# Kernel optimization log

Hardware: AMD Instinct MI355X
Metric: run time of the kernel (lower is better)

## Reference

```python
import jax, jax.numpy as jnp
import numpy as np
import math

B, S, HID = 2, 2048, 1152
NH, NKV = 16, 4
HD = HID // NH  # 72
GROUPS = NH // NKV  # 4
ROPE_BASE = 10000.0


def setup_inputs() -> dict:
    key = jax.random.key(0)
    ks = jax.random.split(key, 5)
    hidden_states = jax.random.normal(ks[0], (B, S, HID), dtype=jnp.float32)
    # causal additive mask: 0 on/below diagonal, -1e9 above
    causal = jnp.tril(jnp.ones((S, S), dtype=jnp.bool_))
    attention_mask = jnp.where(causal, 0.0, -1e9).astype(jnp.float32)[None, None]
    scale = 0.02
    wq = jax.random.normal(ks[1], (HID, HID), dtype=jnp.float32) * scale
    wk = jax.random.normal(ks[2], (NKV * HD, HID), dtype=jnp.float32) * scale
    wv = jax.random.normal(ks[3], (NKV * HD, HID), dtype=jnp.float32) * scale
    wo = jax.random.normal(ks[4], (HID, HID), dtype=jnp.float32) * scale
    return {"hidden_states": hidden_states, "attention_mask": attention_mask,
            "wq": wq, "wk": wk, "wv": wv, "wo": wo}


def _rotate_half(x):
    x1, x2 = jnp.split(x, 2, axis=-1)
    return jnp.concatenate((-x2, x1), axis=-1)


def _rope_cos_sin(seq_len, dim, dtype):
    inv_freq = 1.0 / (ROPE_BASE ** (jnp.arange(0, dim, 2, dtype=jnp.float32) / dim))
    t = jnp.arange(seq_len, dtype=jnp.float32)
    freqs = jnp.outer(t, inv_freq)          # [S, dim/2]
    emb = jnp.concatenate((freqs, freqs), axis=-1)  # [S, dim]
    return jnp.cos(emb).astype(dtype), jnp.sin(emb).astype(dtype)


def reference(hidden_states, attention_mask, wq, wk, wv, wo):
    b, s, _ = hidden_states.shape
    # projections (nn.Linear: x @ W.T)
    q = (hidden_states @ wq.T).reshape(b, s, NH, HD).transpose(0, 2, 1, 3)    # [b,nh,s,hd]
    k = (hidden_states @ wk.T).reshape(b, s, NKV, HD).transpose(0, 2, 1, 3)   # [b,nkv,s,hd]
    v = (hidden_states @ wv.T).reshape(b, s, NKV, HD).transpose(0, 2, 1, 3)
    # RoPE
    cos, sin = _rope_cos_sin(s, HD, hidden_states.dtype)
    cos, sin = cos[None, None], sin[None, None]  # [1,1,s,hd]
    q = q * cos + _rotate_half(q) * sin
    k = k * cos + _rotate_half(k) * sin
    # expand kv heads (repeat_interleave over head dim)
    k = jnp.repeat(k, GROUPS, axis=1)  # [b,nh,s,hd]
    v = jnp.repeat(v, GROUPS, axis=1)
    scores = jnp.einsum('bhqd,bhkd->bhqk', q, k) / math.sqrt(HD)
    scores = scores + attention_mask
    attn = jax.nn.softmax(scores.astype(jnp.float32), axis=-1).astype(q.dtype)
    out = jnp.einsum('bhqk,bhkd->bhqd', attn, v)
    out = out.transpose(0, 2, 1, 3).reshape(b, s, HID)
    return out @ wo.T
```

## Files before the change

### kernel.cpp

```cpp
#include <hip/hip_runtime.h>
#include <hip/hip_bf16.h>
#include <cstddef>

#define B_   2
#define S_   2048
#define HID_ 1152
#define NH_  16
#define NKV_ 4
#define HD_  72
#define MTOT (B_ * S_)
#define KVDIM (NKV_ * HD_)

typedef float f32x4 __attribute__((ext_vector_type(4)));
typedef short bf16x8 __attribute__((ext_vector_type(8)));
typedef short s4v __attribute__((ext_vector_type(4)));

__device__ __forceinline__ float bf2f(short x) {
  unsigned int u = ((unsigned int)(unsigned short)x) << 16;
  return __builtin_bit_cast(float, u);
}
__device__ __forceinline__ short f2bf(float f) {
  unsigned int u = __builtin_bit_cast(unsigned int, f);
  u += 0x7fff + ((u >> 16) & 1);
  return (short)(u >> 16);
}

__device__ __forceinline__ float fast_exp2(float x) {
#if __has_builtin(__builtin_amdgcn_exp2f)
  return __builtin_amdgcn_exp2f(x);
#else
  return exp2f(x);
#endif
}

__device__ __forceinline__ void async16(const short* g, short* lds) {
  __builtin_amdgcn_global_load_lds((const __attribute__((address_space(1))) void*)g,
                                   (__attribute__((address_space(3))) void*)lds,
                                   16, 0, 0);
}

__global__ void k_cvt_all(const float4* __restrict__ s0, const float4* __restrict__ s1,
                          const float4* __restrict__ s2, const float4* __restrict__ s3,
                          const float4* __restrict__ s4,
                          s4v* __restrict__ d0, s4v* __restrict__ d1, s4v* __restrict__ d2,
                          s4v* __restrict__ d3, s4v* __restrict__ d4,
                          float2* __restrict__ tab, short* __restrict__ Vt,
                          int n0, int n1, int n2, int n3, int n4t) {
  int ncvt = n0 + n1 + n2 + n3 + n4t;
  int ntab = S_ * 36;
  int total = ncvt + ntab + 32768;
  for (int i = blockIdx.x * blockDim.x + threadIdx.x; i < total;
       i += gridDim.x * blockDim.x) {
    if (i < ncvt) {
      const float4* s;
      s4v* d;
      int off = i;
      bool perm = false;
      if (off < n0) { s = s0; d = d0; }
      else {
        off -= n0;
        if (off < n1) { s = s1; d = d1; perm = true; }
        else {
          off -= n1;
          if (off < n2) { s = s2; d = d2; perm = true; }
          else {
            off -= n2;
            if (off < n3) { s = s3; d = d3; }
            else { off -= n3; s = s4; d = d4; }
          }
        }
      }
      float4 v = s[off];
      s4v o = { f2bf(v.x), f2bf(v.y), f2bf(v.z), f2bf(v.w) };
      int out = off;
      if (perm) {
        int r = off / 288, k4 = off - r * 288;
        int hh = r / 72, ii = r - hh * 72;
        int pr = hh * 72 + (ii < 36 ? 2 * ii : 2 * (ii - 36) + 1);
        out = pr * 288 + k4;
      }
      d[out] = o;
    } else if (i < ncvt + ntab) {
      int idx = i - ncvt;
      int ii = idx % 36, s = idx / 36;
      float freq = powf(10000.0f, -(float)ii / 36.0f);
      float a = (float)s * freq;
      tab[idx] = make_float2(cosf(a), sinf(a));
    } else {
      int idx2 = i - ncvt - ntab;
      int t = idx2 << 2;
      int sp = t & 2047;
      int rest = t >> 11;
      int dr = rest & 7;
      int bkv = rest >> 3;
      s4v val = {};
      if (dr == 0) { val[0] = (short)0x3F80; val[1] = (short)0x3F80;
                     val[2] = (short)0x3F80; val[3] = (short)0x3F80; }
      *(s4v*)(Vt + (size_t)bkv * 163840 + (size_t)(72 + dr) * 2048 + sp) = val;
    }
  }
}

#define BM 128
#define BN 128
#define BK 32

__global__ __launch_bounds__(256) void k_gemm_qkv(const short* __restrict__ A,
                                                  const short* __restrict__ Wq,
                                                  const short* __restrict__ Wk,
                                                  const short* __restrict__ Wv,
                                                  short* __restrict__ Qo,
                                                  short* __restrict__ Ko,
                                                  short* __restrict__ Vt,
                                                  const float2* __restrict__ tab) {
  const int K = HID_, NTOT = 1728;
  __shared__ short smem[16384];
  short* As0 = smem;
  short* Bs0 = smem + 4096;
  short* As1 = smem + 8192;
  short* Bs1 = smem + 12288;
  const int tid = threadIdx.x;
  const int l = tid & 63;
  const int w = tid >> 6;
  const int bm = blockIdx.x * BM;
  const int bn = blockIdx.y * BN;
  const int wr = (w >> 1) * 64;
  const int wc = (w & 1) * 64;
  const int c15 = l & 15, g = l >> 4;
  const int r0 = tid >> 2;
  const int c0 = (tid & 3) * 8;

  const short* srcA[2];
  const short* srcB[2];
#pragma unroll
  for (int it = 0; it < 2; ++it) {
    int ar = bm + it * 64 + r0;
    int br = bn + it * 64 + r0;
    if (br > NTOT - 1) br = NTOT - 1;
    const short* bsrc;
    if (br < 1152)      bsrc = Wq + (size_t)br * K;
    else if (br < 1440) bsrc = Wk + (size_t)(br - 1152) * K;
    else                bsrc = Wv + (size_t)(br - 1440) * K;
    srcA[it] = A + (size_t)ar * K + c0;
    srcB[it] = bsrc + c0;
  }

  auto STAGE = [&](short* Ad, short* Bd) {
#pragma unroll
    for (int it = 0; it < 2; ++it) {
      async16(srcA[it], &Ad[(it * 64 + r0) * BK + c0]);
      async16(srcB[it], &Bd[(it * 64 + r0) * BK + c0]);
      srcA[it] += BK;
      srcB[it] += BK;
    }
  };

  f32x4 acc[4][4] = {};

  STAGE(As0, Bs0);
  short *Ac = As0, *Bc = Bs0, *An = As1, *Bn = Bs1;

  for (int k0 = 0; k0 < K; k0 += BK) {
    asm volatile("s_waitcnt vmcnt(0)" ::: "memory");
    __builtin_amdgcn_sched_barrier(0);
    __syncthreads();
    if (k0 + BK < K) STAGE(An, Bn);

    bf16x8 af[4], bfr[4];
#pragma unroll
    for (int t = 0; t < 4; ++t) {
      af[t]  = *(const bf16x8*)&Ac[(wr + t * 16 + c15) * BK + g * 8];
      bfr[t] = *(const bf16x8*)&Bc[(wc + t * 16 + c15) * BK + g * 8];
    }
#pragma unroll
    for (int mt = 0; mt < 4; ++mt)
#pragma unroll
      for (int nt = 0; nt < 4; ++nt)
        acc[mt][nt] = __builtin_amdgcn_mfma_f32_16x16x32_bf16(af[mt], bfr[nt], acc[mt][nt], 0, 0, 0);

    short* t1 = Ac; Ac = An; An = t1;
    short* t2 = Bc; Bc = Bn; Bn = t2;
  }

#pragma unroll
  for (int mt = 0; mt < 4; ++mt)
#pragma unroll
    for (int nt = 0; nt < 4; ++nt) {
      int col = bn + wc + nt * 16 + c15;
      if (col < 1152) {
#pragma unroll
        for (int j = 0; j < 4; ++j) {
          int row = bm + wr + mt * 16 + g * 4 + j;
          Qo[(size_t)row * HID_ + col] = f2bf(acc[mt][nt][j]);
        }
      } else if (col < 1440) {
        int ch = col - 1152;
        int ii = (ch % 72) >> 1;
#pragma unroll
        for (int j = 0; j < 4; ++j) {
          int row = bm + wr + mt * 16 + g * 4 + j;
          float v = acc[mt][nt][j];
          float p = __shfl_xor(v, 1);
          float2 cs = tab[(size_t)(row & (S_ - 1)) * 36 + ii];
          float r = (c15 & 1) ? (v * cs.x + p * cs.y)
                              : (v * cs.x - p * cs.y);
          Ko[(size_t)row * KVDIM + ch] = f2bf(r);
        }
      } else if (col < NTOT) {
        int cv = col - 1440;
        int d = cv % 72, kvh = cv / 72;
        int row0 = bm + wr + mt * 16 + g * 4;
        int bkv = (row0 >> 11) * 4 + kvh;
        s4v out;
#pragma unroll
        for (int j = 0; j < 4; ++j) out[j] = f2bf(acc[mt][nt][j]);
        *(s4v*)(Vt + (size_t)bkv * 163840 + (size_t)d * 2048 + (row0 & 2047)) = out;
      }
    }
}

__global__ __launch_bounds__(256) void k_gemm_o(const short* __restrict__ A,
                                                const short* __restrict__ Bm,
                                                float* __restrict__ C,
                                                int M, int N, int K) {
  __shared__ short smem[16384];
  short* As0 = smem;
  short* Bs0 = smem + 4096;
  short* As1 = smem + 8192;
  short* Bs1 = smem + 12288;
  const int tid = threadIdx.x;
  const int l = tid & 63;
  const int w = tid >> 6;
  const int bm = blockIdx.x * BM;
  const int bn = blockIdx.y * BN;
  const int wr = (w >> 1) * 64;
  const int wc = (w & 1) * 64;
  const int c15 = l & 15, g = l >> 4;
  const int r0 = tid >> 2;
  const int c0 = (tid & 3) * 8;

  const short* srcA[2];
  const short* srcB[2];
#pragma unroll
  for (int it = 0; it < 2; ++it) {
    int ar = bm + it * 64 + r0;
    int br = bn + it * 64 + r0;
    if (br > N - 1) br = N - 1;
    srcA[it] = A + (size_t)ar * K + c0;
    srcB[it] = Bm + (size_t)br * K + c0;
  }

  auto STAGE = [&](short* Ad, short* Bd) {
#pragma unroll
    for (int it = 0; it < 2; ++it) {
      async16(srcA[it], &Ad[(it * 64 + r0) * BK + c0]);
      async16(srcB[it], &Bd[(it * 64 + r0) * BK + c0]);
      srcA[it] += BK;
      srcB[it] += BK;
    }
  };

  f32x4 acc[4][4] = {};

  STAGE(As0, Bs0);
  short *Ac = As0, *Bc = Bs0, *An = As1, *Bn = Bs1;

  for (int k0 = 0; k0 < K; k0 += BK) {
    asm volatile("s_waitcnt vmcnt(0)" ::: "memory");
    __builtin_amdgcn_sched_barrier(0);
    __syncthreads();
    if (k0 + BK < K) STAGE(An, Bn);

    bf16x8 af[4], bfr[4];
#pragma unroll
    for (int t = 0; t < 4; ++t) {
      af[t]  = *(const bf16x8*)&Ac[(wr + t * 16 + c15) * BK + g * 8];
      bfr[t] = *(const bf16x8*)&Bc[(wc + t * 16 + c15) * BK + g * 8];
    }
#pragma unroll
    for (int mt = 0; mt < 4; ++mt)
#pragma unroll
      for (int nt = 0; nt < 4; ++nt)
        acc[mt][nt] = __builtin_amdgcn_mfma_f32_16x16x32_bf16(af[mt], bfr[nt], acc[mt][nt], 0, 0, 0);

    short* t1 = Ac; Ac = An; An = t1;
    short* t2 = Bc; Bc = Bn; Bn = t2;
  }

#pragma unroll
  for (int mt = 0; mt < 4; ++mt)
#pragma unroll
    for (int nt = 0; nt < 4; ++nt)
#pragma unroll
      for (int j = 0; j < 4; ++j) {
        int row = bm + wr + mt * 16 + g * 4 + j;
        int col = bn + wc + nt * 16 + c15;
        if (col < N) C[(size_t)row * N + col] = acc[mt][nt][j];
      }
}

#define QB 16
#define KT 64

__global__ __launch_bounds__(256, 2) void k_flash(const short* __restrict__ Q,
                                                  const short* __restrict__ Kg,
                                                  const short* __restrict__ Vt,
                                                  short* __restrict__ O,
                                                  const float2* __restrict__ tab) {
  const int bid = blockIdx.x;
  const int bkv = bid & 7;
  const int qt = 127 - (bid >> 3);
  const int b = bkv >> 2, kv = bkv & 3;
  const int tid = threadIdx.x;
  const int w = tid >> 6, l = tid & 63;
  const int h = kv * 4 + w;
  const int q0 = qt * QB;
  const int c15 = l & 15, g = l >> 4;

  __shared__ short lds[24064];
  short* Ks0 = lds;
  short* Ks1 = lds + 9728;
  short* Ps  = lds + 19456 + w * 1152;

  const float SCL = 0.117851130f * 1.4426950408889634f;
  const float SHIFT = 8.0f;

  const short* Qbase = Q + (size_t)(b * S_) * HID_ + h * HD_;
  const short* Kbase = Kg + (size_t)(b * S_) * KVDIM + kv * HD_;
  const short* Vbase = Vt + (size_t)bkv * 80 * S_;

  const short* gk[3];
  const short* gv[3];
  int lk[3], lv[3];
  bool vkf[3], vvf[3];
#pragma unroll
  for (int i = 0; i < 3; ++i) {
    int c = tid + 256 * i;
    vkf[i] = c < 576;
    int row = c / 9, cc = c - row * 9;
    if (row > 63) row = 63;
    gk[i] = Kbase + (size_t)row * KVDIM + cc * 8;
    lk[i] = c < 576 ? c * 8 : 0;
    int c2 = tid + 256 * i;
    vvf[i] = c2 < 640;
    int vrow = (c2 >> 3) & 127, slot = c2 & 7;
    if (vrow > 79) vrow = 79;
    gv[i] = Vbase + (size_t)vrow * S_ + ((slot ^ (vrow & 7)) << 3);
    lv[i] = c2 < 640 ? c2 * 8 : 0;
  }

  const int lane_k = c15 * 72 + g * 8;
  const short* rKa = Ks0 + lane_k;
  const short* rKb = Ks1 + lane_k;
  const int lane_v0 = 4608 + c15 * 64 + ((g ^ (c15 & 7)) << 3);
  const int lane_v1 = 4608 + c15 * 64 + (((4 + g) ^ (c15 & 7)) << 3);
  const short* rV0a = lds + lane_v0;
  const short* rV0b = lds + 9728 + lane_v0;
  const short* rV1a = lds + lane_v1;
  const short* rV1b = lds + 9728 + lane_v1;
  short* pPw = Ps + g * 288 + c15;
  const short* pPr = Ps + c15 * 72 + g * 8;

  bf16x8 qf[3];
  const bf16x8 zfrag = {0, 0, 0, 0, 0, 0, 0, 0};
  {
    int row = q0 + c15;
    const short* qrow = Qbase + (size_t)row * HID_;
    const float2* trow = tab + (size_t)row * 36;
#pragma unroll
    for (int ks = 0; ks < 3; ++ks) {
      int d0 = ks * 32 + g * 8;
      if (d0 < HD_) {
        bf16x8 raw = *(const bf16x8*)(qrow + d0);
        bf16x8 o;
#pragma unroll
        for (int e = 0; e < 8; e += 2) {
          float2 cs = trow[(d0 + e) >> 1];
          float x1 = bf2f(raw[e]), x2 = bf2f(raw[e + 1]);
          o[e]     = f2bf((x1 * cs.x - x2 * cs.y) * SCL);
          o[e + 1] = f2bf((x2 * cs.x + x1 * cs.y) * SCL);
        }
        qf[ks] = o;
      } else {
        qf[ks] = zfrag;
      }
    }
  }

  f32x4 accO[5] = {};

  const int nkt = (q0 + QB + KT - 1) / KT;
  const int nfull = (QB * qt + 1) >> 6;

  auto STAGE = [&](short* Kd, short* Vd) {
#pragma unroll
    for (int i = 0; i < 3; ++i) {
      if (vkf[i]) async16(gk[i], Kd + lk[i]);
      if (vvf[i]) async16(gv[i], Vd + lv[i]);
      gk[i] += KT * KVDIM;
      gv[i] += KT;
    }
  };

  STAGE(Ks0, lds + 4608);
  const short *rKc = rKa, *rKn = rKb;
  const short *rV0c = rV0a, *rV0n = rV0b;
  const short *rV1c = rV1a, *rV1n = rV1b;
  short *sKn = Ks1, *sVn = lds + 14336;
  short *sKc = Ks0, *sVc = lds + 4608;

  for (int kt = 0; kt < nkt; ++kt) {
    asm volatile("s_waitcnt vmcnt(0)" ::: "memory");
    __builtin_amdgcn_sched_barrier(0);
    __syncthreads();
    if (kt + 1 < nkt) STAGE(sKn, sVn);

    const int kbase = kt * KT;

    f32x4 sc[4] = {};
    __builtin_amdgcn_s_setprio(1);
#pragma unroll
    for (int ct = 0; ct < 4; ++ct)
#pragma unroll
      for (int ks = 0; ks < 3; ++ks) {
        bf16x8 kf = *(const bf16x8*)&rKc[ct * 1152 + ks * 32];
        sc[ct] = __builtin_amdgcn_mfma_f32_16x16x32_bf16(qf[ks], kf, sc[ct], 0, 0, 0);
      }
    __builtin_amdgcn_s_setprio(0);

    const int qrow = q0 + g * 4;
    if (kt >= nfull) {
#pragma unroll
      for (int ct = 0; ct < 4; ++ct) {
        int col = kbase + ct * 16 + c15;
#pragma unroll
        for (int j = 0; j < 4; ++j)
          if (col > qrow + j) sc[ct][j] = -1e30f;
      }
    }
#pragma unroll
    for (int ct = 0; ct < 4; ++ct)
#pragma unroll
      for (int j = 0; j < 4; ++j)
        sc[ct][j] = fast_exp2(sc[ct][j] - SHIFT);

#pragma unroll
    for (int ct = 0; ct < 4; ++ct)
#pragma unroll
      for (int j = 0; j < 4; ++j)
        pPw[j * 72 + ct * 16] = f2bf(sc[ct][j]);
    asm volatile("s_waitcnt lgkmcnt(0)" ::: "memory");
    __builtin_amdgcn_sched_barrier(0);
    bf16x8 pa0 = *(const bf16x8*)&pPr[0];
    bf16x8 pa1 = *(const bf16x8*)&pPr[32];

    __builtin_amdgcn_s_setprio(1);
#pragma unroll
    for (int dt = 0; dt < 5; ++dt) {
      bf16x8 vb0 = *(const bf16x8*)&rV0c[dt * 1024];
      bf16x8 vb1 = *(const bf16x8*)&rV1c[dt * 1024];
      accO[dt] = __builtin_amdgcn_mfma_f32_16x16x32_bf16(pa0, vb0, accO[dt], 0, 0, 0);
      accO[dt] = __builtin_amdgcn_mfma_f32_16x16x32_bf16(pa1, vb1, accO[dt], 0, 0, 0);
    }
    __builtin_amdgcn_s_setprio(0);

    const short* t;
    t = rKc; rKc = rKn; rKn = t;
    t = rV0c; rV0c = rV0n; rV0n = t;
    t = rV1c; rV1c = rV1n; rV1n = t;
    short* ts;
    ts = sKc; sKc = sKn; sKn = ts;
    ts = sVc; sVc = sVn; sVn = ts;
  }

  float lj[4];
#pragma unroll
  for (int j = 0; j < 4; ++j)
    lj[j] = 1.0f / __shfl(accO[4][j], (l & 48) | 8);
#pragma unroll
  for (int dt = 0; dt < 5; ++dt) {
    int d = dt * 16 + c15;
    if (d < HD_) {
#pragma unroll
      for (int j = 0; j < 4; ++j) {
        int row = q0 + g * 4 + j;
        O[(size_t)(b * S_ + row) * HID_ + h * HD_ + d] = f2bf(accO[dt][j] * lj[j]);
      }
    }
  }
}

extern "C" void kernel_launch(void* const* d_in, const int* in_sizes, int n_in,
                              void* d_out, int out_size, void* d_ws, size_t ws_size,
                              hipStream_t stream) {
  const float* hs = (const float*)d_in[0];
  const float* wq = (const float*)d_in[2];
  const float* wk = (const float*)d_in[3];
  const float* wv = (const float*)d_in[4];
  const float* wo = (const float*)d_in[5];

  char* ws = (char*)d_ws;
  short* Xb  = (short*)(ws + 0);
  short* Qb  = (short*)(ws + 9437184);
  short* Kb  = (short*)(ws + 18874368);
  short* Vt  = (short*)(ws + 23592960);
  short* Ob  = (short*)(ws + 26214400);
  short* wqb = (short*)(ws + 35651584);
  short* wkb = (short*)(ws + 38305792);
  short* wvb = (short*)(ws + 38969344);
  short* wob = (short*)(ws + 39632896);
  float2* tab = (float2*)(ws + 42287104);

  k_cvt_all<<<2048, 256, 0, stream>>>(
      (const float4*)hs, (const float4*)wq, (const float4*)wk, (const float4*)wv,
      (const float4*)wo,
      (s4v*)Xb, (s4v*)wqb, (s4v*)wkb, (s4v*)wvb, (s4v*)wob, tab, Vt,
      MTOT * HID_ / 4, HID_ * HID_ / 4, KVDIM * HID_ / 4, KVDIM * HID_ / 4,
      HID_ * HID_ / 4);

  k_gemm_qkv<<<dim3(32, 14), 256, 0, stream>>>(Xb, wqb, wkb, wvb, Qb, Kb, Vt, tab);

  k_flash<<<1024, 256, 0, stream>>>(Qb, Kb, Vt, Ob, tab);

  k_gemm_o<<<dim3(32, 9), 256, 0, stream>>>(Ob, wob, (float*)d_out, MTOT, HID_, HID_);
}
```

Measured before the change: 112.0 us.

## Double flash-attention key tile to 128 and reuse K buffer for probabilities

Raises the key/value tile size in the flash attention kernel from 64 to 128, so each iteration issues twice as many MFMAs per barrier and the loop runs half as many iterations. The P scratch area is dropped and probabilities are written into the just-consumed K tile, with an added __syncthreads before the writes. The V layout swizzle becomes 16-wide for 128-column rows. Staging addresses are recomputed each iteration instead of held in registers. LDS use grows, which may lower occupancy, and the causal tail does more masked wasted work per tile.

```diff
diff --git a/kernel.cpp b/kernel.cpp
--- a/kernel.cpp
+++ b/kernel.cpp
@@ -300,7 +300,7 @@
 }
 
 #define QB 16
-#define KT 64
+#define KT 128
 
 __global__ __launch_bounds__(256, 2) void k_flash(const short* __restrict__ Q,
                                                   const short* __restrict__ Kg,
@@ -317,10 +317,11 @@
   const int q0 = qt * QB;
   const int c15 = l & 15, g = l >> 4;
 
-  __shared__ short lds[24064];
+  __shared__ short lds[38912];
   short* Ks0 = lds;
-  short* Ks1 = lds + 9728;
-  short* Ps  = lds + 19456 + w * 1152;
+  short* Vs0 = lds + 9216;
+  short* Ks1 = lds + 19456;
+  short* Vs1 = lds + 28672;
 
   const float SCL = 0.117851130f * 1.4426950408889634f;
   const float SHIFT = 8.0f;
@@ -329,37 +330,14 @@
   const short* Kbase = Kg + (size_t)(b * S_) * KVDIM + kv * HD_;
   const short* Vbase = Vt + (size_t)bkv * 80 * S_;
 
-  const short* gk[3];
-  const short* gv[3];
-  int lk[3], lv[3];
-  bool vkf[3], vvf[3];
-#pragma unroll
-  for (int i = 0; i < 3; ++i) {
-    int c = tid + 256 * i;
-    vkf[i] = c < 576;
-    int row = c / 9, cc = c - row * 9;
-    if (row > 63) row = 63;
-    gk[i] = Kbase + (size_t)row * KVDIM + cc * 8;
-    lk[i] = c < 576 ? c * 8 : 0;
-    int c2 = tid + 256 * i;
-    vvf[i] = c2 < 640;
-    int vrow = (c2 >> 3) & 127, slot = c2 & 7;
-    if (vrow > 79) vrow = 79;
-    gv[i] = Vbase + (size_t)vrow * S_ + ((slot ^ (vrow & 7)) << 3);
-    lv[i] = c2 < 640 ? c2 * 8 : 0;
-  }
-
   const int lane_k = c15 * 72 + g * 8;
-  const short* rKa = Ks0 + lane_k;
-  const short* rKb = Ks1 + lane_k;
-  const int lane_v0 = 4608 + c15 * 64 + ((g ^ (c15 & 7)) << 3);
-  const int lane_v1 = 4608 + c15 * 64 + (((4 + g) ^ (c15 & 7)) << 3);
-  const short* rV0a = lds + lane_v0;
-  const short* rV0b = lds + 9728 + lane_v0;
-  const short* rV1a = lds + lane_v1;
-  const short* rV1b = lds + 9728 + lane_v1;
-  short* pPw = Ps + g * 288 + c15;
-  const short* pPr = Ps + c15 * 72 + g * 8;
+  int lane_v[4];
+#pragma unroll
+  for (int ks2 = 0; ks2 < 4; ++ks2)
+    lane_v[ks2] = c15 * 128 + (((ks2 * 4 + g) ^ c15) << 3);
+  const int pbase = w * 2176;
+  const int pw_off = pbase + (g * 4) * 136 + c15;
+  const int pr_off = pbase + c15 * 136 + g * 8;
 
   bf16x8 qf[3];
   const bf16x8 zfrag = {0, 0, 0, 0, 0, 0, 0, 0};
@@ -389,41 +367,44 @@
 
   f32x4 accO[5] = {};
 
-  const int nkt = (q0 + QB + KT - 1) / KT;
-  const int nfull = (QB * qt + 1) >> 6;
-
-  auto STAGE = [&](short* Kd, short* Vd) {
-#pragma unroll
-    for (int i = 0; i < 3; ++i) {
-      if (vkf[i]) async16(gk[i], Kd + lk[i]);
-      if (vvf[i]) async16(gv[i], Vd + lv[i]);
-      gk[i] += KT * KVDIM;
-      gv[i] += KT;
+  const int nkt = (16 * qt + 143) >> 7;
+  const int nfull = (16 * qt + 1) >> 7;
+
+  auto STAGE = [&](int kb, short* Kd, short* Vd) {
+    const short* kp = Kbase + (size_t)kb * KVDIM;
+    const short* vp = Vbase + kb;
+#pragma unroll
+    for (int i = 0; i < 10; ++i) {
+      int c = tid + 256 * i;
+      if (c < 1152) {
+        int row = c / 9, cc = c - row * 9;
+        async16(kp + (size_t)row * KVDIM + cc * 8, &Kd[c * 8]);
+      } else if (c < 2432) {
+        int c2 = c - 1152;
+        int row = c2 >> 4, slot = c2 & 15;
+        async16(vp + (size_t)row * S_ + ((slot ^ (row & 15)) << 3), &Vd[c2 * 8]);
+      }
     }
   };
 
-  STAGE(Ks0, lds + 4608);
-  const short *rKc = rKa, *rKn = rKb;
-  const short *rV0c = rV0a, *rV0n = rV0b;
-  const short *rV1c = rV1a, *rV1n = rV1b;
-  short *sKn = Ks1, *sVn = lds + 14336;
-  short *sKc = Ks0, *sVc = lds + 4608;
+  STAGE(0, Ks0, Vs0);
+  short *Ksc = Ks0, *Vsc = Vs0, *Ksn = Ks1, *Vsn = Vs1;
 
   for (int kt = 0; kt < nkt; ++kt) {
     asm volatile("s_waitcnt vmcnt(0)" ::: "memory");
     __builtin_amdgcn_sched_barrier(0);
     __syncthreads();
-    if (kt + 1 < nkt) STAGE(sKn, sVn);
+    if (kt + 1 < nkt) STAGE((kt + 1) * KT, Ksn, Vsn);
 
     const int kbase = kt * KT;
 
-    f32x4 sc[4] = {};
+    f32x4 sc[8] = {};
     __builtin_amdgcn_s_setprio(1);
 #pragma unroll
-    for (int ct = 0; ct < 4; ++ct)
+    for (int ct = 0; ct < 8; ++ct)
 #pragma unroll
       for (int ks = 0; ks < 3; ++ks) {
-        bf16x8 kf = *(const bf16x8*)&rKc[ct * 1152 + ks * 32];
+        bf16x8 kf = *(const bf16x8*)&Ksc[lane_k + ct * 1152 + ks * 32];
         sc[ct] = __builtin_amdgcn_mfma_f32_16x16x32_bf16(qf[ks], kf, sc[ct], 0, 0, 0);
       }
     __builtin_amdgcn_s_setprio(0);
@@ -431,7 +412,7 @@
     const int qrow = q0 + g * 4;
     if (kt >= nfull) {
 #pragma unroll
-      for (int ct = 0; ct < 4; ++ct) {
+      for (int ct = 0; ct < 8; ++ct) {
         int col = kbase + ct * 16 + c15;
 #pragma unroll
         for (int j = 0; j < 4; ++j)
@@ -439,38 +420,37 @@
       }
     }
 #pragma unroll
-    for (int ct = 0; ct < 4; ++ct)
+    for (int ct = 0; ct < 8; ++ct)
 #pragma unroll
       for (int j = 0; j < 4; ++j)
         sc[ct][j] = fast_exp2(sc[ct][j] - SHIFT);
 
-#pragma unroll
-    for (int ct = 0; ct < 4; ++ct)
+    __syncthreads();
+#pragma unroll
+    for (int ct = 0; ct < 8; ++ct)
 #pragma unroll
       for (int j = 0; j < 4; ++j)
-        pPw[j * 72 + ct * 16] = f2bf(sc[ct][j]);
+        Ksc[pw_off + j * 136 + ct * 16] = f2bf(sc[ct][j]);
     asm volatile("s_waitcnt lgkmcnt(0)" ::: "memory");
     __builtin_amdgcn_sched_barrier(0);
-    bf16x8 pa0 = *(const bf16x8*)&pPr[0];
-    bf16x8 pa1 = *(const bf16x8*)&pPr[32];
+    bf16x8 pa[4];
+#pragma unroll
+    for (int ks2 = 0; ks2 < 4; ++ks2)
+      pa[ks2] = *(const bf16x8*)&Ksc[pr_off + ks2 * 32];
 
     __builtin_amdgcn_s_setprio(1);
 #pragma unroll
     for (int dt = 0; dt < 5; ++dt) {
-      bf16x8 vb0 = *(const bf16x8*)&rV0c[dt * 1024];
-      bf16x8 vb1 = *(const bf16x8*)&rV1c[dt * 1024];
-      accO[dt] = __builtin_amdgcn_mfma_f32_16x16x32_bf16(pa0, vb0, accO[dt], 0, 0, 0);
-      accO[dt] = __builtin_amdgcn_mfma_f32_16x16x32_bf16(pa1, vb1, accO[dt], 0, 0, 0);
+#pragma unroll
+      for (int ks2 = 0; ks2 < 4; ++ks2) {
+        bf16x8 vb = *(const bf16x8*)&Vsc[lane_v[ks2] + dt * 2048];
+        accO[dt] = __builtin_amdgcn_mfma_f32_16x16x32_bf16(pa[ks2], vb, accO[dt], 0, 0, 0);
+      }
     }
     __builtin_amdgcn_s_setprio(0);
 
-    const short* t;
-    t = rKc; rKc = rKn; rKn = t;
-    t = rV0c; rV0c = rV0n; rV0n = t;
-    t = rV1c; rV1c = rV1n; rV1n = t;
-    short* ts;
-    ts = sKc; sKc = sKn; sKn = ts;
-    ts = sVc; sVc = sVn; sVn = ts;
+    short* t1 = Ksc; Ksc = Ksn; Ksn = t1;
+    short* t2 = Vsc; Vsc = Vsn; Vsn = t2;
   }
 
   float lj[4];
```

After: 109.5 us. 2.2% less time.
